# Performance work log

Hardware: AMD Instinct MI355X
Metric: run time of the kernel (lower is better)

Reference implementation:

```python
import jax, jax.numpy as jnp
import numpy as np

D = 128   # query_token_dim = tgt_token_dim = qk_dim = v_dim (code constraints)
NH = 8
HD = D // NH
SCALE = HD ** -0.5
B = 4096  # BH1W1: number of cost-map query locations
H0, W0 = 12, 18  # target token spatial size (H3, W3)


def _ln(x, g, b, eps=1e-5):
    m = x.mean(-1, keepdims=True)
    v = ((x - m) ** 2).mean(-1, keepdims=True)
    return (x - m) * jax.lax.rsqrt(v + eps) * g + b


def _broad_attn(q1, kw, vw):
    # q1: [D] single query broadcast across batch; kw, vw: [B, L, D]
    Bq, L, _ = kw.shape
    qh = q1.reshape(NH, HD)
    kh = kw.reshape(Bq, L, NH, HD)
    vh = vw.reshape(Bq, L, NH, HD)
    a = jax.nn.softmax(jnp.einsum('hd,blhd->bhl', qh, kh) * SCALE, axis=-1)
    return jnp.einsum('bhl,blhd->bhd', a, vh).reshape(Bq, D)


def _forward(query, tgt_token, ln1_g, ln1_b, ln2_g, ln2_b, wq, bq, wk, bk, wv, bv,
             wp, bp, f1w, f1b, f2w, f2b, cw, cb,
             ln1c_g, ln1c_b, ln2c_g, ln2c_b, wqc, bqc, wkc, bkc, wvc, bvc,
             wpc, bpc, f1cw, f1cb, f2cw, f2cb, H, W):
    Bq = tgt_token.shape[0]
    sc = query  # [1, 10, D]
    # ---- fine branch: 6 windows (2x3 grid) over full-res target tokens ----
    qn = _ln(query[:, :6, :], ln1_g, ln1_b)
    q = (qn @ wq + bq)[0]                                   # [6, D]
    k = (tgt_token @ wk + bk).reshape(Bq, H, W, D)
    v = (tgt_token @ wv + bv).reshape(Bq, H, W, D)
    hs = [(0, H // 2), (H // 2, H)]
    ws = [(0, W // 3), (W // 3, 2 * (W // 3)), (2 * (W // 3), W)]
    wins = [(h0, h1, w0, w1) for (h0, h1) in hs for (w0, w1) in ws]
    outs = [_broad_attn(q[i],
                        k[:, h0:h1, w0:w1].reshape(Bq, -1, D),
                        v[:, h0:h1, w0:w1].reshape(Bq, -1, D))
            for i, (h0, h1, w0, w1) in enumerate(wins)]
    x = jnp.stack(outs, axis=1)                             # [B, 6, D]
    x = sc[:, :6, :] + (x @ wp + bp)
    xn = _ln(x, ln2_g, ln2_b)
    x_fine = x + (jax.nn.gelu(xn @ f1w + f1b, approximate=False) @ f2w + f2b)
    # ---- coarse branch: 3x3/s2 conv downsample, 4 windows (2x2 grid) ----
    tc = jax.lax.conv_general_dilated(tgt_token.reshape(Bq, H, W, D), cw,
                                      (2, 2), ((1, 1), (1, 1)),
                                      dimension_numbers=('NHWC', 'HWIO', 'NHWC')) + cb
    Hc, Wc = tc.shape[1], tc.shape[2]
    qn = _ln(sc[:, 6:10, :], ln1c_g, ln1c_b)
    qc = (qn @ wqc + bqc)[0]                                # [4, D]
    kc = tc @ wkc + bkc
    vc = tc @ wvc + bvc
    hs = [(0, Hc // 2), (Hc // 2, Hc)]
    ws = [(0, Wc // 2), (Wc // 2, Wc)]
    wins = [(h0, h1, w0, w1) for (h0, h1) in hs for (w0, w1) in ws]
    outs = [_broad_attn(qc[i],
                        kc[:, h0:h1, w0:w1].reshape(Bq, -1, D),
                        vc[:, h0:h1, w0:w1].reshape(Bq, -1, D))
            for i, (h0, h1, w0, w1) in enumerate(wins)]
    x = jnp.stack(outs, axis=1)                             # [B, 4, D]
    x = sc[:, 6:10, :] + (x @ wpc + bpc)
    xn = _ln(x, ln2c_g, ln2c_b)
    x_coarse = x + (jax.nn.gelu(xn @ f1cw + f1cb, approximate=False) @ f2cw + f2cb)
    return jnp.concatenate([x_fine, x_coarse], axis=1)      # [B, 10, D]


def setup_inputs():
    key = jax.random.key(0)
    ks = jax.random.split(key, 16)
    def w(k, shape):
        return jax.random.normal(k, shape, jnp.float32) * 0.05
    z = jnp.zeros((D,), jnp.float32)
    o = jnp.ones((D,), jnp.float32)
    return dict(
        query=jax.random.normal(ks[0], (1, 10, D), jnp.float32),
        tgt_token=jax.random.normal(ks[1], (B, H0 * W0, D), jnp.float32),
        ln1_g=o, ln1_b=z, ln2_g=o, ln2_b=z,
        wq=w(ks[2], (D, D)), bq=z, wk=w(ks[3], (D, D)), bk=z,
        wv=w(ks[4], (D, D)), bv=z, wp=w(ks[5], (D, D)), bp=z,
        f1w=w(ks[6], (D, D)), f1b=z, f2w=w(ks[7], (D, D)), f2b=z,
        cw=w(ks[8], (3, 3, D, D)), cb=z,
        ln1c_g=o, ln1c_b=z, ln2c_g=o, ln2c_b=z,
        wqc=w(ks[9], (D, D)), bqc=z, wkc=w(ks[10], (D, D)), bkc=z,
        wvc=w(ks[11], (D, D)), bvc=z, wpc=w(ks[12], (D, D)), bpc=z,
        f1cw=w(ks[13], (D, D)), f1cb=z, f2cw=w(ks[14], (D, D)), f2cb=z,
        H=H0, W=W0,
    )


def reference(query, tgt_token, ln1_g, ln1_b, ln2_g, ln2_b, wq, bq, wk, bk, wv, bv,
              wp, bp, f1w, f1b, f2w, f2b, cw, cb,
              ln1c_g, ln1c_b, ln2c_g, ln2c_b, wqc, bqc, wkc, bkc, wvc, bvc,
              wpc, bpc, f1cw, f1cb, f2cw, f2cb, H, W):
    return _forward(query, tgt_token, ln1_g, ln1_b, ln2_g, ln2_b, wq, bq, wk, bk,
                    wv, bv, wp, bp, f1w, f1b, f2w, f2b, cw, cb,
                    ln1c_g, ln1c_b, ln2c_g, ln2c_b, wqc, bqc, wkc, bkc, wvc, bvc,
                    wpc, bpc, f1cw, f1cb, f2cw, f2cb, H, W)
```

## Files before the change

kernel.cpp:

```cpp
#include <hip/hip_runtime.h>
#include <math.h>


typedef short   mfrag  __attribute__((ext_vector_type(8)));
typedef float   floatx4 __attribute__((ext_vector_type(4)));
typedef unsigned short us4 __attribute__((ext_vector_type(4)));
typedef unsigned short us8 __attribute__((ext_vector_type(8)));

#define LL   216
#define LC   54
#define TP1  136
#define TP2  72

__device__ __forceinline__ float b2f(unsigned short u){
  return __uint_as_float(((unsigned int)u) << 16);
}
__device__ __forceinline__ unsigned short f2b(float f){
  unsigned int x = __float_as_uint(f);
  return (unsigned short)((x + 0x7fffu + ((x >> 16) & 1u)) >> 16);
}
__device__ __forceinline__ floatx4 mfma16(mfrag a, mfrag b, floatx4 c){
  return __builtin_amdgcn_mfma_f32_16x16x32_bf16(a, b, c, 0, 0, 0);
}
__device__ __forceinline__ mfrag zfrag(){ mfrag z = {0,0,0,0,0,0,0,0}; return z; }

union F8 { unsigned short u[8]; mfrag v; };

struct Par {
  const float *query,*tgt,*ln1g,*ln1b,*ln2g,*ln2b,*wq,*bq,*wk,*wv,*bv,
              *wp,*bp,*f1w,*f1b,*f2w,*f2b,*cw,*cb;
  const float *ln1cg,*ln1cb,*ln2cg,*ln2cb,*wqc,*bqc,*wkc,*wvc,*bvc,
              *wpc,*bpc,*f1cw,*f1cb,*f2cw,*f2cb;
  unsigned short *U;
  float          *uc;
  float          *cvb;
  unsigned short *G;
  unsigned short *cwvT;
  unsigned short *wT;
  float          *out;
};

__global__ __launch_bounds__(256) void kprep(Par p){
  __shared__ __align__(16) unsigned char sm[66048];
  int bid = blockIdx.x, tid = threadIdx.x;
  if (bid > 0){
    float* lt = (float*)sm;
    int slot = bid - 1;
    const float* src;
    switch(slot){ case 0: src=p.wp;  break; case 1: src=p.f1w;  break;
                  case 2: src=p.f2w; break; case 3: src=p.wpc;  break;
                  case 4: src=p.f1cw;break; case 5: src=p.f2cw; break;
                  case 6: src=p.wv;  break; default: src=p.wvc; }
    unsigned short* dst = p.wT + slot*16384;
    for (int o=tid;o<16384;o+=256){ int k=o>>7, n=o&127; lt[n*129+k] = src[o]; }
    __syncthreads();
    for (int o=tid;o<16384;o+=256){ int n=o>>7, k=o&127; dst[o] = f2b(lt[n*129+k]); }
    return;
  }
  float* qn = (float*)sm;
  float* qp = (float*)(sm + 5120);
  unsigned short* wkb = (unsigned short*)(sm + 10240);
  if (tid < 10){
    int r = tid;
    const float* row = p.query + r*128;
    float s1=0.f, s2=0.f;
    for (int c=0;c<128;c++){ float v=row[c]; s1+=v; s2+=v*v; }
    float m = s1/128.f, var = s2/128.f - m*m;
    float inv = rsqrtf(var + 1e-5f);
    const float* g  = (r<6)? p.ln1g : p.ln1cg;
    const float* bb = (r<6)? p.ln1b : p.ln1cb;
    for (int c=0;c<128;c++) qn[r*128+c] = (row[c]-m)*inv*g[c] + bb[c];
  }
  __syncthreads();
  for (int o=tid;o<1280;o+=256){
    int i=o>>7, d=o&127;
    const float* w  = (i<6)? p.wq : p.wqc;
    const float* bi = (i<6)? p.bq : p.bqc;
    float acc = bi[d];
    for (int c=0;c<128;c++) acc += qn[i*128+c]*w[c*128+d];
    qp[i*128+d]=acc;
  }
  if (tid < 128){
    int d = tid; float a = p.bvc[d];
    for (int c=0;c<128;c++) a += p.cb[c] * p.wvc[c*128+d];
    p.cvb[d] = a;
  }
  __syncthreads();
  for (int o=tid;o<16384;o+=256) wkb[(o>>7)*130 + (o&127)] = f2b(p.wk[o]);
  __syncthreads();
  for (int o=tid;o<6144;o+=256){
    int ih=o>>7, c=o&127, i=ih>>3, h=ih&7;
    float a=0.f;
    #pragma unroll
    for (int dd=0;dd<16;dd++) a += b2f(wkb[c*130 + h*16+dd]) * qp[i*128 + h*16+dd];
    p.U[ih*128+c] = f2b(0.25f*a);
  }
  __syncthreads();
  for (int o=tid;o<16384;o+=256) wkb[(o>>7)*130 + (o&127)] = f2b(p.wkc[o]);
  __syncthreads();
  for (int o=tid;o<4096;o+=256){
    int ih=o>>7, c=o&127, i=ih>>3, h=ih&7;
    float a=0.f;
    #pragma unroll
    for (int dd=0;dd<16;dd++) a += b2f(wkb[c*130 + h*16+dd]) * qp[(6+i)*128 + h*16+dd];
    p.uc[ih*128+c] = 0.25f*a;
  }
}

__global__ __launch_bounds__(256) void kfold(Par p){
  __shared__ alignas(16) unsigned short cwb[128*136];
  __shared__ alignas(16) unsigned short ucb[32*136];
  int bid=blockIdx.x, tid=threadIdx.x;
  int lane=tid&63, w=tid>>6, q4=lane>>4, n16=lane&15;
  int tap = (bid<9)? bid : bid-9;
  for (int o=tid;o<16384;o+=256)
    cwb[(o>>7)*136 + (o&127)] = f2b(p.cw[(size_t)tap*16384 + o]);
  if (bid < 9){
    for (int o=tid;o<4096;o+=256) ucb[(o>>7)*136 + (o&127)] = f2b(p.uc[o]);
    __syncthreads();
    #pragma unroll
    for (int nt2=0;nt2<2;nt2++){
      int nt = w + nt2*4;
      #pragma unroll
      for (int mt=0;mt<2;mt++){
        floatx4 acc={0.f,0.f,0.f,0.f};
        #pragma unroll
        for (int ks=0;ks<4;ks++){
          mfrag a  = *reinterpret_cast<const mfrag*>(ucb + (mt*16+n16)*136 + ks*32+q4*8);
          mfrag bf = *reinterpret_cast<const mfrag*>(cwb + (nt*16+n16)*136 + ks*32+q4*8);
          acc = mfma16(a, bf, acc);
        }
        #pragma unroll
        for (int r=0;r<4;r++){
          int ih = mt*16+q4*4+r, e = nt*16+n16;
          p.G[(tap*32+ih)*128 + e] = f2b(acc[r]);
        }
      }
    }
  } else {
    __syncthreads();
    const unsigned short* wvcT = p.wT + 7*16384;
    #pragma unroll 1
    for (int mt=0;mt<8;mt++){
      #pragma unroll
      for (int nt2=0;nt2<2;nt2++){
        int nt = w + nt2*4;
        floatx4 acc={0.f,0.f,0.f,0.f};
        #pragma unroll
        for (int ks=0;ks<4;ks++){
          mfrag a  = *reinterpret_cast<const mfrag*>(cwb + (mt*16+n16)*136 + ks*32+q4*8);
          mfrag bf = *reinterpret_cast<const mfrag*>(wvcT + (nt*16+n16)*128 + ks*32+q4*8);
          acc = mfma16(a, bf, acc);
        }
        us4 pk = { f2b(acc[0]), f2b(acc[1]), f2b(acc[2]), f2b(acc[3]) };
        *reinterpret_cast<us4*>(p.cwvT + ((size_t)tap*128 + nt*16+n16)*128 + mt*16 + q4*4) = pk;
      }
    }
  }
}

__global__ __launch_bounds__(512, 4) void kmain(Par p){
  __shared__ __align__(16) unsigned char smem[81184];
  unsigned short* tile  = (unsigned short*)smem;
  unsigned short* rmap  = (unsigned short*)(smem + 55552);
  unsigned short* rmapF = (unsigned short*)(smem + 56704);
  unsigned char*  regn  = smem + 57472;
  float*          sfT   = (float*)regn;
  unsigned short* aw    = (unsigned short*)(regn + 13056);
  unsigned short* rbA   = (unsigned short*)regn;
  float*          sctT  = (float*)(regn + 13056);
  unsigned short* ba    = (unsigned short*)(regn + 20992);
  unsigned short* ac    = (unsigned short*)regn;
  unsigned char*  vcT   = regn + 4608;
  unsigned short* xb    = (unsigned short*)regn;
  unsigned short* bbq   = (unsigned short*)(regn + 2720);
  unsigned short* hb    = (unsigned short*)(regn + 5440);

  int tid  = threadIdx.x;
  int b    = blockIdx.x;
  int lane = tid & 63, wvx = tid >> 6;
  int q4   = lane >> 4, n16 = lane & 15;
  const float* tb = p.tgt + (size_t)b*LL*128;
  const unsigned char* tB = (const unsigned char*)tile;

  auto tfragX = [&](unsigned ax, int kb)->mfrag {
    return *reinterpret_cast<const mfrag*>(
        tB + ((ax ^ (unsigned)(kb & 0x70)) + (unsigned)(kb & 0xFFFFFF8F)));
  };

  {
    int c4 = tid & 31;
    unsigned c8m = (unsigned)((c4*8) & 0x70), c8l = (unsigned)((c4*8) & 0x88);
    for (int o = tid; o < 217*32; o += 512){
      int row = o >> 5;
      float4 v = make_float4(0.f,0.f,0.f,0.f);
      if (row < 216) v = *reinterpret_cast<const float4*>(tb + row*128 + (c4<<2));
      us4 wv4 = { f2b(v.x), f2b(v.y), f2b(v.z), f2b(v.w) };
      unsigned s = (unsigned)((row & 7) << 4);
      unsigned addr = (unsigned)(row*256) + ((c8m ^ s) + c8l);
      *reinterpret_cast<us4*>((unsigned char*)tile + addr) = wv4;
    }
  }
  for (int o = tid; o < 960; o += 512){
    int row;
    if (o < 576){
      int tap = o >> 6, pos = o & 63;
      int ip = pos/9, jp = pos - ip*9;
      int r = ip*2 + tap/3 - 1, c = jp*2 + (tap%3) - 1;
      row = (pos < 54 && r >= 0 && r < 12 && c >= 0 && c < 18) ? (r*18 + c) : 216;
      rmap[o] = (unsigned short)(row*256 + ((row&7)<<4));
    } else {
      int t = o - 576; int win = t >> 6, lw = t & 63;
      int r0 = (win/3)*6, c0 = (win%3)*6;
      row = (lw < 36) ? ((r0 + lw/6)*18 + c0 + lw%6) : 216;
      rmapF[t] = (unsigned short)(row*256 + ((row&7)<<4));
    }
  }
  __syncthreads();

  for (int task = wvx; task < 18; task += 8){
    int win = task/3, rg = task - win*3;
    unsigned ax = rmapF[win*64 + rg*16 + n16];
    floatx4 acc = {0.f,0.f,0.f,0.f};
    #pragma unroll
    for (int ks=0; ks<4; ks++){
      mfrag a = tfragX(ax, ks*64 + q4*16);
      mfrag bf = zfrag();
      if (n16 < 8) bf = *reinterpret_cast<const mfrag*>(p.U + (win*8+n16)*128 + ks*32 + q4*8);
      acc = mfma16(a, bf, acc);
    }
    if (n16 < 8){
      #pragma unroll
      for (int r=0;r<4;r++){
        int l = rg*16 + q4*4 + r;
        if (l < 36) sfT[(win*8+n16)*40 + l] = acc[r];
      }
    }
  }
  __syncthreads();
  {
    int l = lane;
    for (int rr=0; rr<6; rr++){
      int row = wvx*6 + rr;
      float v = (l < 36) ? sfT[row*40 + l] : -1e30f;
      float mx = v;
      #pragma unroll
      for (int m=1;m<64;m<<=1) mx = fmaxf(mx, __shfl_xor(mx, m));
      float e = (l < 36) ? __expf(v - mx) : 0.f;
      float sm = e;
      #pragma unroll
      for (int m=1;m<64;m<<=1) sm += __shfl_xor(sm, m);
      aw[row*TP2 + l] = f2b(e * (1.f/sm));
    }
  }
  __syncthreads();
  {
    int nt = wvx;
    unsigned c2 = (unsigned)((nt*16 + n16)*2);
    unsigned c2m = c2 & 0x70u, c2l = c2 & 0x8Fu;
    for (int win=0; win<6; win++){
      floatx4 acc={0.f,0.f,0.f,0.f};
      #pragma unroll
      for (int ks=0; ks<2; ks++){
        mfrag a = zfrag();
        if (n16 < 8) a = *reinterpret_cast<const mfrag*>(aw + (win*8+n16)*TP2 + ks*32 + q4*8);
        us8 rv = *reinterpret_cast<const us8*>(rmapF + win*64 + ks*32 + q4*8);
        F8 bb;
        #pragma unroll
        for (int j=0;j<8;j++)
          bb.u[j] = *reinterpret_cast<const unsigned short*>(tB + (((unsigned)rv[j] ^ c2m) + c2l));
        acc = mfma16(a, bb.v, acc);
      }
      #pragma unroll
      for (int r=0;r<4;r++){
        int h = q4*4 + r;
        if (h < 8) rbA[(win*8+h)*TP1 + nt*16 + n16] = f2b(acc[r]);
      }
    }
  }
  __syncthreads();
  {
    int h = wvx;
    const unsigned short* wvT = p.wT + 6*16384;
    floatx4 acc = {0.f,0.f,0.f,0.f};
    #pragma unroll
    for (int ks=0; ks<4; ks++){
      mfrag a = zfrag();
      if (n16 < 6) a = *reinterpret_cast<const mfrag*>(rbA + (n16*8+h)*TP1 + ks*32 + q4*8);
      mfrag bf = *reinterpret_cast<const mfrag*>(wvT + (h*16+n16)*128 + ks*32 + q4*8);
      acc = mfma16(a, bf, acc);
    }
    float bvd = p.bv[h*16+n16];
    #pragma unroll
    for (int r=0;r<4;r++){
      int win = q4*4 + r;
      if (win < 6) ba[win*TP1 + h*16 + n16] = f2b(acc[r] + bvd);
    }
  }
  {
    int g = wvx >> 1, nt = wvx & 1;
    int pos = g*16 + n16;
    floatx4 acc = {0.f,0.f,0.f,0.f};
    for (int tap=0; tap<9; tap++){
      unsigned ax = rmap[tap*64 + pos];
      #pragma unroll
      for (int ks=0; ks<4; ks++){
        mfrag a = tfragX(ax, ks*64 + q4*16);
        mfrag bf = *reinterpret_cast<const mfrag*>(
            p.G + (size_t)(tap*32 + nt*16 + n16)*128 + ks*32 + q4*8);
        acc = mfma16(a, bf, acc);
      }
    }
    #pragma unroll
    for (int r=0;r<4;r++){
      int l = g*16 + q4*4 + r;
      if (l < LC) sctT[(nt*16+n16)*56 + l] = acc[r];
    }
  }
  __syncthreads();
  {
    int l = lane;
    int rl = (l < 54) ? (l/9) : 0, cl = (l < 54) ? (l - (l/9)*9) : 0;
    for (int rr=0; rr<4; rr++){
      int ih = wvx*4 + rr;
      int i = ih >> 3;
      int rA = (i>>1)*3, cA = (i&1)*4, cB = (i&1)? 9 : 4;
      bool member = (l < 54) && rl >= rA && rl < rA+3 && cl >= cA && cl < cB;
      float s = member ? sctT[ih*56 + l] : -1e30f;
      float mx = s;
      #pragma unroll
      for (int m=1;m<64;m<<=1) mx = fmaxf(mx, __shfl_xor(mx, m));
      float e = member ? __expf(s - mx) : 0.f;
      float sm = e;
      #pragma unroll
      for (int m=1;m<64;m<<=1) sm += __shfl_xor(sm, m);
      ac[ih*TP2 + l] = f2b(e * (1.f/sm));
    }
  }
  __syncthreads();
  {
    int dt = wvx;
    floatx4 va0={0.f,0.f,0.f,0.f}, va1={0.f,0.f,0.f,0.f},
            va2={0.f,0.f,0.f,0.f}, va3={0.f,0.f,0.f,0.f};
    for (int tap=0; tap<9; tap++){
      unsigned ax0 = rmap[tap*64 +  0 + n16];
      unsigned ax1 = rmap[tap*64 + 16 + n16];
      unsigned ax2 = rmap[tap*64 + 32 + n16];
      unsigned ax3 = rmap[tap*64 + 48 + n16];
      const unsigned short* cwp = p.cwvT + ((size_t)tap*128 + dt*16 + n16)*128;
      #pragma unroll
      for (int ks=0; ks<4; ks++){
        mfrag bf = *reinterpret_cast<const mfrag*>(cwp + ks*32 + q4*8);
        va0 = mfma16(tfragX(ax0, ks*64 + q4*16), bf, va0);
        va1 = mfma16(tfragX(ax1, ks*64 + q4*16), bf, va1);
        va2 = mfma16(tfragX(ax2, ks*64 + q4*16), bf, va2);
        va3 = mfma16(tfragX(ax3, ks*64 + q4*16), bf, va3);
      }
    }
    int d = dt*16 + n16;
    unsigned drow = (unsigned)(d*128), dsw = (unsigned)((d & 7) << 4);
    us4 p0 = { f2b(va0[0]), f2b(va0[1]), f2b(va0[2]), f2b(va0[3]) };
    us4 p1 = { f2b(va1[0]), f2b(va1[1]), f2b(va1[2]), f2b(va1[3]) };
    us4 p2 = { f2b(va2[0]), f2b(va2[1]), f2b(va2[2]), f2b(va2[3]) };
    us4 p3 = { f2b(va3[0]), f2b(va3[1]), f2b(va3[2]), f2b(va3[3]) };
    *reinterpret_cast<us4*>(vcT + drow + ((unsigned)( 0 + q4*8) ^ dsw)) = p0;
    *reinterpret_cast<us4*>(vcT + drow + ((unsigned)(32 + q4*8) ^ dsw)) = p1;
    *reinterpret_cast<us4*>(vcT + drow + ((unsigned)(64 + q4*8) ^ dsw)) = p2;
    *reinterpret_cast<us4*>(vcT + drow + ((unsigned)(96 + q4*8) ^ dsw)) = p3;
  }
  __syncthreads();
  {
    int nt = wvx, d = nt*16 + n16;
    unsigned dsw = (unsigned)((d & 7) << 4);
    floatx4 pa0={0.f,0.f,0.f,0.f}, pa1={0.f,0.f,0.f,0.f};
    #pragma unroll
    for (int ks=0; ks<2; ks++){
      mfrag bf = *reinterpret_cast<const mfrag*>(
          vcT + (unsigned)(d*128) + ((unsigned)(ks*64 + q4*16) ^ dsw));
      mfrag a0 = *reinterpret_cast<const mfrag*>(ac + n16*TP2        + ks*32 + q4*8);
      mfrag a1 = *reinterpret_cast<const mfrag*>(ac + (16+n16)*TP2   + ks*32 + q4*8);
      pa0 = mfma16(a0, bf, pa0);
      pa1 = mfma16(a1, bf, pa1);
    }
    float cvbd = p.cvb[d];
    float s0 = 0.f, s1 = 0.f;
    #pragma unroll
    for (int r=0;r<4;r++) if ((nt&3)==r){ s0 = pa0[r]; s1 = pa1[r]; }
    int q_lo = nt>>2, q_hi = q_lo + 2;
    if (q4 == q_lo){ ba[6*TP1 + d] = f2b(s0 + cvbd); ba[8*TP1 + d] = f2b(s1 + cvbd); }
    if (q4 == q_hi){ ba[7*TP1 + d] = f2b(s0 + cvbd); ba[9*TP1 + d] = f2b(s1 + cvbd); }
  }
  __syncthreads();
  {
    int nt = wvx, d = nt*16 + n16;
    const unsigned short* wF = p.wT + 0*16384;
    const unsigned short* wC = p.wT + 3*16384;
    floatx4 aF={0.f,0.f,0.f,0.f}, aC={0.f,0.f,0.f,0.f};
    #pragma unroll
    for (int ks=0;ks<4;ks++){
      mfrag vF = zfrag(), vC = zfrag();
      if (n16 < 6)       vF = *reinterpret_cast<const mfrag*>(ba + n16*TP1 + ks*32+q4*8);
      else if (n16 < 10) vC = *reinterpret_cast<const mfrag*>(ba + n16*TP1 + ks*32+q4*8);
      mfrag BF = *reinterpret_cast<const mfrag*>(wF + (nt*16+n16)*128 + ks*32+q4*8);
      mfrag BC = *reinterpret_cast<const mfrag*>(wC + (nt*16+n16)*128 + ks*32+q4*8);
      aF = mfma16(vF, BF, aF);
      aC = mfma16(vC, BC, aC);
    }
    float bF = p.bp[d], bC = p.bpc[d];
    #pragma unroll
    for (int r=0;r<4;r++){
      int m = q4*4+r;
      if (m < 6)            xb[m*TP1+d] = f2b(aF[r] + bF + p.query[m*128+d]);
      else if (m < 10)      xb[m*TP1+d] = f2b(aC[r] + bC + p.query[m*128+d]);
    }
  }
  __syncthreads();
  for (int row = wvx; row < 10; row += 8){
    bool fine = row < 6;
    const float* g2 = fine? p.ln2g : p.ln2cg;
    const float* e2 = fine? p.ln2b : p.ln2cb;
    float v0 = b2f(xb[row*TP1 + lane]), v1 = b2f(xb[row*TP1 + 64 + lane]);
    float s = v0+v1, sq = v0*v0+v1*v1;
    #pragma unroll
    for (int m=1;m<64;m<<=1){ s += __shfl_xor(s, m); sq += __shfl_xor(sq, m); }
    float mean = s*(1.f/128.f), var = sq*(1.f/128.f) - mean*mean;
    float inv = rsqrtf(var + 1e-5f);
    bbq[row*TP1 + lane]      = f2b((v0-mean)*inv*g2[lane] + e2[lane]);
    bbq[row*TP1 + 64 + lane] = f2b((v1-mean)*inv*g2[64+lane] + e2[64+lane]);
  }
  __syncthreads();
  {
    int nt = wvx, d = nt*16 + n16;
    const unsigned short* wF = p.wT + 1*16384;
    const unsigned short* wC = p.wT + 4*16384;
    floatx4 aF={0.f,0.f,0.f,0.f}, aC={0.f,0.f,0.f,0.f};
    #pragma unroll
    for (int ks=0;ks<4;ks++){
      mfrag vF = zfrag(), vC = zfrag();
      if (n16 < 6)       vF = *reinterpret_cast<const mfrag*>(bbq + n16*TP1 + ks*32+q4*8);
      else if (n16 < 10) vC = *reinterpret_cast<const mfrag*>(bbq + n16*TP1 + ks*32+q4*8);
      mfrag BF = *reinterpret_cast<const mfrag*>(wF + (nt*16+n16)*128 + ks*32+q4*8);
      mfrag BC = *reinterpret_cast<const mfrag*>(wC + (nt*16+n16)*128 + ks*32+q4*8);
      aF = mfma16(vF, BF, aF);
      aC = mfma16(vC, BC, aC);
    }
    float bF = p.f1b[d], bC = p.f1cb[d];
    #pragma unroll
    for (int r=0;r<4;r++){
      int m = q4*4+r;
      float v;
      if (m < 6) v = aF[r] + bF;
      else       v = aC[r] + bC;
      if (m < 10) hb[m*TP1+d] = f2b(0.5f*v*(1.f+erff(v*0.70710678118f)));
    }
  }
  __syncthreads();
  {
    int nt = wvx, d = nt*16 + n16;
    const unsigned short* wF = p.wT + 2*16384;
    const unsigned short* wC = p.wT + 5*16384;
    floatx4 aF={0.f,0.f,0.f,0.f}, aC={0.f,0.f,0.f,0.f};
    #pragma unroll
    for (int ks=0;ks<4;ks++){
      mfrag vF = zfrag(), vC = zfrag();
      if (n16 < 6)       vF = *reinterpret_cast<const mfrag*>(hb + n16*TP1 + ks*32+q4*8);
      else if (n16 < 10) vC = *reinterpret_cast<const mfrag*>(hb + n16*TP1 + ks*32+q4*8);
      mfrag BF = *reinterpret_cast<const mfrag*>(wF + (nt*16+n16)*128 + ks*32+q4*8);
      mfrag BC = *reinterpret_cast<const mfrag*>(wC + (nt*16+n16)*128 + ks*32+q4*8);
      aF = mfma16(vF, BF, aF);
      aC = mfma16(vC, BC, aC);
    }
    float bF = p.f2b[d], bC = p.f2cb[d];
    #pragma unroll
    for (int r=0;r<4;r++){
      int m = q4*4+r;
      if (m < 10){
        float accv = (m < 6) ? (aF[r] + bF) : (aC[r] + bC);
        p.out[((size_t)b*10 + m)*128 + d] = b2f(xb[m*TP1+d]) + accv;
      }
    }
  }
}

extern "C" void kernel_launch(void* const* d_in, const int* in_sizes, int n_in,
                              void* d_out, int out_size, void* d_ws, size_t ws_size,
                              hipStream_t stream){
  (void)in_sizes; (void)n_in; (void)out_size; (void)ws_size;
  Par p;
  p.query=(const float*)d_in[0];  p.tgt  =(const float*)d_in[1];
  p.ln1g =(const float*)d_in[2];  p.ln1b =(const float*)d_in[3];
  p.ln2g =(const float*)d_in[4];  p.ln2b =(const float*)d_in[5];
  p.wq   =(const float*)d_in[6];  p.bq   =(const float*)d_in[7];
  p.wk   =(const float*)d_in[8];
  p.wv   =(const float*)d_in[10]; p.bv   =(const float*)d_in[11];
  p.wp   =(const float*)d_in[12]; p.bp   =(const float*)d_in[13];
  p.f1w  =(const float*)d_in[14]; p.f1b  =(const float*)d_in[15];
  p.f2w  =(const float*)d_in[16]; p.f2b  =(const float*)d_in[17];
  p.cw   =(const float*)d_in[18]; p.cb   =(const float*)d_in[19];
  p.ln1cg=(const float*)d_in[20]; p.ln1cb=(const float*)d_in[21];
  p.ln2cg=(const float*)d_in[22]; p.ln2cb=(const float*)d_in[23];
  p.wqc  =(const float*)d_in[24]; p.bqc  =(const float*)d_in[25];
  p.wkc  =(const float*)d_in[26];
  p.wvc  =(const float*)d_in[28]; p.bvc  =(const float*)d_in[29];
  p.wpc  =(const float*)d_in[30]; p.bpc  =(const float*)d_in[31];
  p.f1cw =(const float*)d_in[32]; p.f1cb =(const float*)d_in[33];
  p.f2cw =(const float*)d_in[34]; p.f2cb =(const float*)d_in[35];
  char* ws = (char*)d_ws;
  p.U    = (unsigned short*)(ws + 0);
  p.uc   = (float*)        (ws + 16384);
  p.cvb  = (float*)        (ws + 32768);
  p.G    = (unsigned short*)(ws + 33280);
  p.cwvT = (unsigned short*)(ws + 107008);
  p.wT   = (unsigned short*)(ws + 401920);
  p.out  = (float*)d_out;

  kprep<<<dim3(9),    dim3(256), 0, stream>>>(p);
  kfold<<<dim3(18),   dim3(256), 0, stream>>>(p);
  kmain<<<dim3(4096), dim3(512), 0, stream>>>(p);
}
```

Measured before the change: 1.113 ms.

## Pre-swizzle weight operands into MFMA fragment order and rebalance conv-V tiling

Stores all bf16 weight matrices (wT, U, G, cwvT) in MFMA-fragment-major layout so each lane loads its 8 operand values as one contiguous 16-byte chunk, giving fully coalesced global loads inside the main kernel. The per-window U operand is zero-padded to 16 columns so the conditional load is dropped. The coarse value-conv GEMM now uses a 2x2 register tile (two position groups by two output tiles) instead of 1x4, which changes operand reuse. The prep work is also split across an extra block, with fine and coarse query projections computed in parallel.

```diff
diff --git a/kernel.cpp b/kernel.cpp
--- a/kernel.cpp
+++ b/kernel.cpp
@@ -25,6 +25,7 @@
 __device__ __forceinline__ mfrag zfrag(){ mfrag z = {0,0,0,0,0,0,0,0}; return z; }
 
 union F8 { unsigned short u[8]; mfrag v; };
+
 
 struct Par {
   const float *query,*tgt,*ln1g,*ln1b,*ln2g,*ln2b,*wq,*bq,*wk,*wv,*bv,
@@ -43,7 +44,7 @@
 __global__ __launch_bounds__(256) void kprep(Par p){
   __shared__ __align__(16) unsigned char sm[66048];
   int bid = blockIdx.x, tid = threadIdx.x;
-  if (bid > 0){
+  if (bid >= 1 && bid <= 8){
     float* lt = (float*)sm;
     int slot = bid - 1;
     const float* src;
@@ -51,59 +52,80 @@
                   case 2: src=p.f2w; break; case 3: src=p.wpc;  break;
                   case 4: src=p.f1cw;break; case 5: src=p.f2cw; break;
                   case 6: src=p.wv;  break; default: src=p.wvc; }
-    unsigned short* dst = p.wT + slot*16384;
     for (int o=tid;o<16384;o+=256){ int k=o>>7, n=o&127; lt[n*129+k] = src[o]; }
     __syncthreads();
-    for (int o=tid;o<16384;o+=256){ int n=o>>7, k=o&127; dst[o] = f2b(lt[n*129+k]); }
+    for (int o=tid;o<16384;o+=256){
+      int n=o>>7, k=o&127;
+      int idx = ((slot*8 + (n>>4))*4 + (k>>5))*512
+              + ((k>>3)&3)*128 + (n&15)*8 + (k&7);
+      p.wT[idx] = f2b(lt[n*129+k]);
+    }
     return;
   }
   float* qn = (float*)sm;
   float* qp = (float*)(sm + 5120);
   unsigned short* wkb = (unsigned short*)(sm + 10240);
-  if (tid < 10){
-    int r = tid;
-    const float* row = p.query + r*128;
-    float s1=0.f, s2=0.f;
-    for (int c=0;c<128;c++){ float v=row[c]; s1+=v; s2+=v*v; }
-    float m = s1/128.f, var = s2/128.f - m*m;
-    float inv = rsqrtf(var + 1e-5f);
-    const float* g  = (r<6)? p.ln1g : p.ln1cg;
-    const float* bb = (r<6)? p.ln1b : p.ln1cb;
-    for (int c=0;c<128;c++) qn[r*128+c] = (row[c]-m)*inv*g[c] + bb[c];
-  }
-  __syncthreads();
-  for (int o=tid;o<1280;o+=256){
-    int i=o>>7, d=o&127;
-    const float* w  = (i<6)? p.wq : p.wqc;
-    const float* bi = (i<6)? p.bq : p.bqc;
-    float acc = bi[d];
-    for (int c=0;c<128;c++) acc += qn[i*128+c]*w[c*128+d];
-    qp[i*128+d]=acc;
-  }
-  if (tid < 128){
-    int d = tid; float a = p.bvc[d];
-    for (int c=0;c<128;c++) a += p.cb[c] * p.wvc[c*128+d];
-    p.cvb[d] = a;
-  }
-  __syncthreads();
-  for (int o=tid;o<16384;o+=256) wkb[(o>>7)*130 + (o&127)] = f2b(p.wk[o]);
-  __syncthreads();
-  for (int o=tid;o<6144;o+=256){
-    int ih=o>>7, c=o&127, i=ih>>3, h=ih&7;
-    float a=0.f;
-    #pragma unroll
-    for (int dd=0;dd<16;dd++) a += b2f(wkb[c*130 + h*16+dd]) * qp[i*128 + h*16+dd];
-    p.U[ih*128+c] = f2b(0.25f*a);
-  }
-  __syncthreads();
-  for (int o=tid;o<16384;o+=256) wkb[(o>>7)*130 + (o&127)] = f2b(p.wkc[o]);
-  __syncthreads();
-  for (int o=tid;o<4096;o+=256){
-    int ih=o>>7, c=o&127, i=ih>>3, h=ih&7;
-    float a=0.f;
-    #pragma unroll
-    for (int dd=0;dd<16;dd++) a += b2f(wkb[c*130 + h*16+dd]) * qp[(6+i)*128 + h*16+dd];
-    p.uc[ih*128+c] = 0.25f*a;
+  if (bid == 0){
+    if (tid < 6){
+      int r = tid;
+      const float* row = p.query + r*128;
+      float s1=0.f, s2=0.f;
+      for (int c=0;c<128;c++){ float v=row[c]; s1+=v; s2+=v*v; }
+      float m = s1/128.f, var = s2/128.f - m*m;
+      float inv = rsqrtf(var + 1e-5f);
+      for (int c=0;c<128;c++) qn[r*128+c] = (row[c]-m)*inv*p.ln1g[c] + p.ln1b[c];
+    }
+    for (int o=tid;o<12288;o+=256) p.U[o] = 0;
+    if (tid < 128){
+      int d = tid; float a = p.bvc[d];
+      for (int c=0;c<128;c++) a += p.cb[c] * p.wvc[c*128+d];
+      p.cvb[d] = a;
+    }
+    __syncthreads();
+    for (int o=tid;o<768;o+=256){
+      int i=o>>7, d=o&127;
+      float acc = p.bq[d];
+      for (int c=0;c<128;c++) acc += qn[i*128+c]*p.wq[c*128+d];
+      qp[i*128+d]=acc;
+    }
+    __syncthreads();
+    for (int o=tid;o<16384;o+=256) wkb[(o>>7)*130 + (o&127)] = f2b(p.wk[o]);
+    __syncthreads();
+    for (int o=tid;o<6144;o+=256){
+      int ih=o>>7, c=o&127, i=ih>>3, h=ih&7;
+      float a=0.f;
+      #pragma unroll
+      for (int dd=0;dd<16;dd++) a += b2f(wkb[c*130 + h*16+dd]) * qp[i*128 + h*16+dd];
+      int idx = (i*4 + (c>>5))*512 + ((c>>3)&3)*128 + h*8 + (c&7);
+      p.U[idx] = f2b(0.25f*a);
+    }
+  } else {
+    if (tid >= 6 && tid < 10){
+      int r = tid;
+      const float* row = p.query + r*128;
+      float s1=0.f, s2=0.f;
+      for (int c=0;c<128;c++){ float v=row[c]; s1+=v; s2+=v*v; }
+      float m = s1/128.f, var = s2/128.f - m*m;
+      float inv = rsqrtf(var + 1e-5f);
+      for (int c=0;c<128;c++) qn[r*128+c] = (row[c]-m)*inv*p.ln1cg[c] + p.ln1cb[c];
+    }
+    __syncthreads();
+    for (int o=tid;o<512;o+=256){
+      int i=6+(o>>7), d=o&127;
+      float acc = p.bqc[d];
+      for (int c=0;c<128;c++) acc += qn[i*128+c]*p.wqc[c*128+d];
+      qp[i*128+d]=acc;
+    }
+    __syncthreads();
+    for (int o=tid;o<16384;o+=256) wkb[(o>>7)*130 + (o&127)] = f2b(p.wkc[o]);
+    __syncthreads();
+    for (int o=tid;o<4096;o+=256){
+      int ih=o>>7, c=o&127, i=ih>>3, h=ih&7;
+      float a=0.f;
+      #pragma unroll
+      for (int dd=0;dd<16;dd++) a += b2f(wkb[c*130 + h*16+dd]) * qp[(6+i)*128 + h*16+dd];
+      p.uc[ih*128+c] = 0.25f*a;
+    }
   }
 }
 
@@ -132,14 +154,14 @@
         }
         #pragma unroll
         for (int r=0;r<4;r++){
-          int ih = mt*16+q4*4+r, e = nt*16+n16;
-          p.G[(tap*32+ih)*128 + e] = f2b(acc[r]);
+          int idx = ((tap*2+mt)*4 + (nt>>1))*512
+                  + ((nt&1)*2 + (n16>>3))*128 + (q4*4+r)*8 + (n16&7);
+          p.G[idx] = f2b(acc[r]);
         }
       }
     }
   } else {
     __syncthreads();
-    const unsigned short* wvcT = p.wT + 7*16384;
     #pragma unroll 1
     for (int mt=0;mt<8;mt++){
       #pragma unroll
@@ -149,11 +171,13 @@
         #pragma unroll
         for (int ks=0;ks<4;ks++){
           mfrag a  = *reinterpret_cast<const mfrag*>(cwb + (mt*16+n16)*136 + ks*32+q4*8);
-          mfrag bf = *reinterpret_cast<const mfrag*>(wvcT + (nt*16+n16)*128 + ks*32+q4*8);
+          mfrag bf = *reinterpret_cast<const mfrag*>(p.wT + ((7*8+nt)*4+ks)*512 + lane*8);
           acc = mfma16(a, bf, acc);
         }
+        size_t base = (size_t)((tap*8+nt)*4 + (mt>>1))*512
+                    + ((mt&1)*2 + (q4>>1))*128 + n16*8 + (q4&1)*4;
         us4 pk = { f2b(acc[0]), f2b(acc[1]), f2b(acc[2]), f2b(acc[3]) };
-        *reinterpret_cast<us4*>(p.cwvT + ((size_t)tap*128 + nt*16+n16)*128 + mt*16 + q4*4) = pk;
+        *reinterpret_cast<us4*>(p.cwvT + base) = pk;
       }
     }
   }
@@ -225,8 +249,7 @@
     #pragma unroll
     for (int ks=0; ks<4; ks++){
       mfrag a = tfragX(ax, ks*64 + q4*16);
-      mfrag bf = zfrag();
-      if (n16 < 8) bf = *reinterpret_cast<const mfrag*>(p.U + (win*8+n16)*128 + ks*32 + q4*8);
+      mfrag bf = *reinterpret_cast<const mfrag*>(p.U + (win*4+ks)*512 + lane*8);
       acc = mfma16(a, bf, acc);
     }
     if (n16 < 8){
@@ -281,13 +304,12 @@
   __syncthreads();
   {
     int h = wvx;
-    const unsigned short* wvT = p.wT + 6*16384;
     floatx4 acc = {0.f,0.f,0.f,0.f};
     #pragma unroll
     for (int ks=0; ks<4; ks++){
       mfrag a = zfrag();
       if (n16 < 6) a = *reinterpret_cast<const mfrag*>(rbA + (n16*8+h)*TP1 + ks*32 + q4*8);
-      mfrag bf = *reinterpret_cast<const mfrag*>(wvT + (h*16+n16)*128 + ks*32 + q4*8);
+      mfrag bf = *reinterpret_cast<const mfrag*>(p.wT + ((6*8+h)*4+ks)*512 + lane*8);
       acc = mfma16(a, bf, acc);
     }
     float bvd = p.bv[h*16+n16];
@@ -306,8 +328,7 @@
       #pragma unroll
       for (int ks=0; ks<4; ks++){
         mfrag a = tfragX(ax, ks*64 + q4*16);
-        mfrag bf = *reinterpret_cast<const mfrag*>(
-            p.G + (size_t)(tap*32 + nt*16 + n16)*128 + ks*32 + q4*8);
+        mfrag bf = *reinterpret_cast<const mfrag*>(p.G + ((tap*2+nt)*4+ks)*512 + lane*8);
         acc = mfma16(a, bf, acc);
       }
     }
@@ -339,34 +360,39 @@
   }
   __syncthreads();
   {
-    int dt = wvx;
-    floatx4 va0={0.f,0.f,0.f,0.f}, va1={0.f,0.f,0.f,0.f},
-            va2={0.f,0.f,0.f,0.f}, va3={0.f,0.f,0.f,0.f};
+    int g2 = wvx & 1, dq = wvx >> 1;
+    floatx4 a00={0.f,0.f,0.f,0.f}, a01={0.f,0.f,0.f,0.f},
+            a10={0.f,0.f,0.f,0.f}, a11={0.f,0.f,0.f,0.f};
     for (int tap=0; tap<9; tap++){
-      unsigned ax0 = rmap[tap*64 +  0 + n16];
-      unsigned ax1 = rmap[tap*64 + 16 + n16];
-      unsigned ax2 = rmap[tap*64 + 32 + n16];
-      unsigned ax3 = rmap[tap*64 + 48 + n16];
-      const unsigned short* cwp = p.cwvT + ((size_t)tap*128 + dt*16 + n16)*128;
+      unsigned axA = rmap[tap*64 + (g2*2+0)*16 + n16];
+      unsigned axB = rmap[tap*64 + (g2*2+1)*16 + n16];
+      const unsigned short* c0 = p.cwvT + (size_t)((tap*8 + dq*2+0)*4)*512;
+      const unsigned short* c1 = p.cwvT + (size_t)((tap*8 + dq*2+1)*4)*512;
       #pragma unroll
       for (int ks=0; ks<4; ks++){
-        mfrag bf = *reinterpret_cast<const mfrag*>(cwp + ks*32 + q4*8);
-        va0 = mfma16(tfragX(ax0, ks*64 + q4*16), bf, va0);
-        va1 = mfma16(tfragX(ax1, ks*64 + q4*16), bf, va1);
-        va2 = mfma16(tfragX(ax2, ks*64 + q4*16), bf, va2);
-        va3 = mfma16(tfragX(ax3, ks*64 + q4*16), bf, va3);
-      }
-    }
-    int d = dt*16 + n16;
-    unsigned drow = (unsigned)(d*128), dsw = (unsigned)((d & 7) << 4);
-    us4 p0 = { f2b(va0[0]), f2b(va0[1]), f2b(va0[2]), f2b(va0[3]) };
-    us4 p1 = { f2b(va1[0]), f2b(va1[1]), f2b(va1[2]), f2b(va1[3]) };
-    us4 p2 = { f2b(va2[0]), f2b(va2[1]), f2b(va2[2]), f2b(va2[3]) };
-    us4 p3 = { f2b(va3[0]), f2b(va3[1]), f2b(va3[2]), f2b(va3[3]) };
-    *reinterpret_cast<us4*>(vcT + drow + ((unsigned)( 0 + q4*8) ^ dsw)) = p0;
-    *reinterpret_cast<us4*>(vcT + drow + ((unsigned)(32 + q4*8) ^ dsw)) = p1;
-    *reinterpret_cast<us4*>(vcT + drow + ((unsigned)(64 + q4*8) ^ dsw)) = p2;
-    *reinterpret_cast<us4*>(vcT + drow + ((unsigned)(96 + q4*8) ^ dsw)) = p3;
+        mfrag fa0 = tfragX(axA, ks*64 + q4*16);
+        mfrag fa1 = tfragX(axB, ks*64 + q4*16);
+        mfrag fb0 = *reinterpret_cast<const mfrag*>(c0 + ks*512 + lane*8);
+        mfrag fb1 = *reinterpret_cast<const mfrag*>(c1 + ks*512 + lane*8);
+        a00 = mfma16(fa0, fb0, a00);
+        a01 = mfma16(fa0, fb1, a01);
+        a10 = mfma16(fa1, fb0, a10);
+        a11 = mfma16(fa1, fb1, a11);
+      }
+    }
+    #pragma unroll
+    for (int pg=0; pg<2; pg++){
+      #pragma unroll
+      for (int dt2=0; dt2<2; dt2++){
+        floatx4 av = pg ? (dt2 ? a11 : a10) : (dt2 ? a01 : a00);
+        int d = (dq*2+dt2)*16 + n16;
+        int pos0 = (g2*2+pg)*16 + q4*4;
+        unsigned addr = (unsigned)(d*128)
+                      + (((unsigned)(pos0*2)) ^ ((unsigned)((d&7)<<4)));
+        us4 pk = { f2b(av[0]), f2b(av[1]), f2b(av[2]), f2b(av[3]) };
+        *reinterpret_cast<us4*>(vcT + addr) = pk;
+      }
+    }
   }
   __syncthreads();
   {
@@ -377,10 +403,10 @@
     for (int ks=0; ks<2; ks++){
       mfrag bf = *reinterpret_cast<const mfrag*>(
           vcT + (unsigned)(d*128) + ((unsigned)(ks*64 + q4*16) ^ dsw));
-      mfrag a0 = *reinterpret_cast<const mfrag*>(ac + n16*TP2        + ks*32 + q4*8);
-      mfrag a1 = *reinterpret_cast<const mfrag*>(ac + (16+n16)*TP2   + ks*32 + q4*8);
-      pa0 = mfma16(a0, bf, pa0);
-      pa1 = mfma16(a1, bf, pa1);
+      mfrag fa0 = *reinterpret_cast<const mfrag*>(ac + n16*TP2        + ks*32 + q4*8);
+      mfrag fa1 = *reinterpret_cast<const mfrag*>(ac + (16+n16)*TP2   + ks*32 + q4*8);
+      pa0 = mfma16(fa0, bf, pa0);
+      pa1 = mfma16(fa1, bf, pa1);
     }
     float cvbd = p.cvb[d];
     float s0 = 0.f, s1 = 0.f;
@@ -393,16 +419,14 @@
   __syncthreads();
   {
     int nt = wvx, d = nt*16 + n16;
-    const unsigned short* wF = p.wT + 0*16384;
-    const unsigned short* wC = p.wT + 3*16384;
     floatx4 aF={0.f,0.f,0.f,0.f}, aC={0.f,0.f,0.f,0.f};
     #pragma unroll
     for (int ks=0;ks<4;ks++){
       mfrag vF = zfrag(), vC = zfrag();
       if (n16 < 6)       vF = *reinterpret_cast<const mfrag*>(ba + n16*TP1 + ks*32+q4*8);
       else if (n16 < 10) vC = *reinterpret_cast<const mfrag*>(ba + n16*TP1 + ks*32+q4*8);
-      mfrag BF = *reinterpret_cast<const mfrag*>(wF + (nt*16+n16)*128 + ks*32+q4*8);
-      mfrag BC = *reinterpret_cast<const mfrag*>(wC + (nt*16+n16)*128 + ks*32+q4*8);
+      mfrag BF = *reinterpret_cast<const mfrag*>(p.wT + ((0*8+nt)*4+ks)*512 + lane*8);
+      mfrag BC = *reinterpret_cast<const mfrag*>(p.wT + ((3*8+nt)*4+ks)*512 + lane*8);
       aF = mfma16(vF, BF, aF);
       aC = mfma16(vC, BC, aC);
     }
@@ -417,7 +441,7 @@
   __syncthreads();
   for (int row = wvx; row < 10; row += 8){
     bool fine = row < 6;
-    const float* g2 = fine? p.ln2g : p.ln2cg;
+    const float* g2v = fine? p.ln2g : p.ln2cg;
     const float* e2 = fine? p.ln2b : p.ln2cb;
     float v0 = b2f(xb[row*TP1 + lane]), v1 = b2f(xb[row*TP1 + 64 + lane]);
     float s = v0+v1, sq = v0*v0+v1*v1;
@@ -425,22 +449,20 @@
     for (int m=1;m<64;m<<=1){ s += __shfl_xor(s, m); sq += __shfl_xor(sq, m); }
     float mean = s*(1.f/128.f), var = sq*(1.f/128.f) - mean*mean;
     float inv = rsqrtf(var + 1e-5f);
-    bbq[row*TP1 + lane]      = f2b((v0-mean)*inv*g2[lane] + e2[lane]);
-    bbq[row*TP1 + 64 + lane] = f2b((v1-mean)*inv*g2[64+lane] + e2[64+lane]);
+    bbq[row*TP1 + lane]      = f2b((v0-mean)*inv*g2v[lane] + e2[lane]);
+    bbq[row*TP1 + 64 + lane] = f2b((v1-mean)*inv*g2v[64+lane] + e2[64+lane]);
   }
   __syncthreads();
   {
     int nt = wvx, d = nt*16 + n16;
-    const unsigned short* wF = p.wT + 1*16384;
-    const unsigned short* wC = p.wT + 4*16384;
     floatx4 aF={0.f,0.f,0.f,0.f}, aC={0.f,0.f,0.f,0.f};
     #pragma unroll
     for (int ks=0;ks<4;ks++){
       mfrag vF = zfrag(), vC = zfrag();
       if (n16 < 6)       vF = *reinterpret_cast<const mfrag*>(bbq + n16*TP1 + ks*32+q4*8);
       else if (n16 < 10) vC = *reinterpret_cast<const mfrag*>(bbq + n16*TP1 + ks*32+q4*8);
-      mfrag BF = *reinterpret_cast<const mfrag*>(wF + (nt*16+n16)*128 + ks*32+q4*8);
-      mfrag BC = *reinterpret_cast<const mfrag*>(wC + (nt*16+n16)*128 + ks*32+q4*8);
+      mfrag BF = *reinterpret_cast<const mfrag*>(p.wT + ((1*8+nt)*4+ks)*512 + lane*8);
+      mfrag BC = *reinterpret_cast<const mfrag*>(p.wT + ((4*8+nt)*4+ks)*512 + lane*8);
       aF = mfma16(vF, BF, aF);
       aC = mfma16(vC, BC, aC);
     }
@@ -457,16 +479,14 @@
   __syncthreads();
   {
     int nt = wvx, d = nt*16 + n16;
-    const unsigned short* wF = p.wT + 2*16384;
-    const unsigned short* wC = p.wT + 5*16384;
     floatx4 aF={0.f,0.f,0.f,0.f}, aC={0.f,0.f,0.f,0.f};
     #pragma unroll
     for (int ks=0;ks<4;ks++){
       mfrag vF = zfrag(), vC = zfrag();
       if (n16 < 6)       vF = *reinterpret_cast<const mfrag*>(hb + n16*TP1 + ks*32+q4*8);
       else if (n16 < 10) vC = *reinterpret_cast<const mfrag*>(hb + n16*TP1 + ks*32+q4*8);
-      mfrag BF = *reinterpret_cast<const mfrag*>(wF + (nt*16+n16)*128 + ks*32+q4*8);
-      mfrag BC = *reinterpret_cast<const mfrag*>(wC + (nt*16+n16)*128 + ks*32+q4*8);
+      mfrag BF = *reinterpret_cast<const mfrag*>(p.wT + ((2*8+nt)*4+ks)*512 + lane*8);
+      mfrag BC = *reinterpret_cast<const mfrag*>(p.wT + ((5*8+nt)*4+ks)*512 + lane*8);
       aF = mfma16(vF, BF, aF);
       aC = mfma16(vC, BC, aC);
     }
@@ -507,14 +527,14 @@
   p.f2cw =(const float*)d_in[34]; p.f2cb =(const float*)d_in[35];
   char* ws = (char*)d_ws;
   p.U    = (unsigned short*)(ws + 0);
-  p.uc   = (float*)        (ws + 16384);
-  p.cvb  = (float*)        (ws + 32768);
-  p.G    = (unsigned short*)(ws + 33280);
-  p.cwvT = (unsigned short*)(ws + 107008);
-  p.wT   = (unsigned short*)(ws + 401920);
+  p.uc   = (float*)        (ws + 24576);
+  p.cvb  = (float*)        (ws + 40960);
+  p.G    = (unsigned short*)(ws + 41472);
+  p.cwvT = (unsigned short*)(ws + 115200);
+  p.wT   = (unsigned short*)(ws + 410112);
   p.out  = (float*)d_out;
 
-  kprep<<<dim3(9),    dim3(256), 0, stream>>>(p);
+  kprep<<<dim3(10),   dim3(256), 0, stream>>>(p);
   kfold<<<dim3(18),   dim3(256), 0, stream>>>(p);
   kmain<<<dim3(4096), dim3(512), 0, stream>>>(p);
 }
```

After: 998.7 us. -10.3%, faster.
